# Performance work log

Measured on AMD Instinct MI355X. Metric: run time of the kernel, lower is better.

## Reference

```python
import jax, jax.numpy as jnp
import numpy as np

K = 1024
T = 16384
P = 2          # number of lags
N_STAGES = 2   # len(s_list)
EDGE_P = 0.005 # edge density -> avg degree ~5


def setup_inputs() -> dict:
    key = jax.random.key(0)
    kX, kA, ka, kb0, kb1 = jax.random.split(key, 5)
    X = jax.random.normal(kX, (K, T), dtype=jnp.float32)
    # sparse symmetric 0/1 adjacency, zero diagonal
    U = jax.random.uniform(kA, (K, K))
    Ab = (U < EDGE_P)
    Ab = (Ab | Ab.T) & ~jnp.eye(K, dtype=bool)
    A = Ab.astype(jnp.float32)
    alpha = jax.random.normal(ka, (P,), dtype=jnp.float32)
    beta0 = jax.random.normal(kb0, (P,), dtype=jnp.float32)
    beta1 = jax.random.normal(kb1, (P,), dtype=jnp.float32)
    return {"X": X, "A": A, "alpha": alpha, "beta0": beta0, "beta1": beta1}


def _stage_avg_matrices(A):
    """M[r] averages over nodes at shortest-path distance exactly r+1 (rows with
    no stage-r neighbors are all-zero, matching the `if neighbors:` guard)."""
    Ab = A > 0.5
    Af = Ab.astype(jnp.float32)
    reach_prev = jnp.eye(A.shape[0], dtype=bool)  # distance <= 0
    Ms = []
    for _ in range(N_STAGES):
        reach = reach_prev | ((reach_prev.astype(jnp.float32) @ Af) > 0.5)
        exact = reach & ~reach_prev                     # distance == r+1
        exact_f = exact.astype(jnp.float32)
        deg = exact_f.sum(axis=1, keepdims=True)        # (K, 1)
        M = exact_f / jnp.maximum(deg, 1.0)             # zero rows stay zero
        Ms.append(M)
        reach_prev = reach
    return Ms


def reference(X, A, alpha, beta0, beta1):
    K_, T_ = X.shape
    betas = [beta0, beta1]
    Ms = _stage_avg_matrices(A)
    # one dense aggregation per stage over ALL time steps, then slice lags
    MXs = [M @ X for M in Ms]                           # each (K, T)
    Y = jnp.zeros((K_, T_ - P), dtype=X.dtype)
    for lag in range(1, P + 1):
        sl = slice(P - lag, T_ - lag)
        Y = Y + alpha[lag - 1] * X[:, sl]
        for stage in range(N_STAGES):
            Y = Y + betas[stage][lag - 1] * MXs[stage][:, sl]
    return Y
```

## Files before the change

kernel.cpp:

```cpp
#include <hip/hip_runtime.h>

typedef float fx4 __attribute__((ext_vector_type(4)));
typedef short s16x8 __attribute__((ext_vector_type(8)));
typedef __bf16 bfx8 __attribute__((ext_vector_type(8)));

#define KN 1024
#define TT 16384
#define NOUT 16382
#define NKT 32
#define COLP 16640
#define HLDS 49216

#define APK_OFF 34078720u
#define B1_OFF  (APK_OFF + 4194304u)

__device__ __forceinline__ unsigned short f2bf(float f) {
  return __builtin_bit_cast(unsigned short, (__bf16)f);
}

__device__ __forceinline__ void gll16(const void* g, void* l) {
  __builtin_amdgcn_global_load_lds(
      (const __attribute__((address_space(1))) void*)g,
      (__attribute__((address_space(3))) void*)l, 16, 0, 0);
}

__global__ __launch_bounds__(256) void k_masks(const float* __restrict__ A,
                                               unsigned* __restrict__ B1) {
  int k = blockIdx.x;
  int tid = threadIdx.x;
  int wv = tid >> 6, lane = tid & 63;
  for (int i = 0; i < 4; ++i) {
    int n = i * 256 + wv * 64 + lane;
    bool bit = (A[(size_t)k * KN + n] > 0.5f) && (n != k);
    unsigned long long m = __ballot(bit);
    if (lane == 0) {
      B1[k * 32 + i * 8 + wv * 2]     = (unsigned)m;
      B1[k * 32 + i * 8 + wv * 2 + 1] = (unsigned)(m >> 32);
    }
  }
}

__global__ __launch_bounds__(256) void k_wp(const unsigned* __restrict__ B1,
                                            const float* __restrict__ alpha,
                                            const float* __restrict__ beta0,
                                            const float* __restrict__ beta1,
                                            const float* __restrict__ X,
                                            unsigned short* __restrict__ Wc,
                                            unsigned short* __restrict__ Xbf) {
  int tid = threadIdx.x;
  if (blockIdx.x >= 1024) {
    int p = blockIdx.x - 1024;
    int o = p & 127;
    int cb = p >> 7;
    int c = cb * 256 + tid;
    unsigned v[4];
#pragma unroll
    for (int q = 0; q < 4; ++q) {
      float f0 = 0.f, f1 = 0.f;
      if (c < TT) {
        f0 = X[(size_t)(o * 8 + q * 2) * TT + c];
        f1 = X[(size_t)(o * 8 + q * 2 + 1) * TT + c];
      }
      v[q] = (unsigned)f2bf(f0) | ((unsigned)f2bf(f1) << 16);
    }
    uint4 w; w.x = v[0]; w.y = v[1]; w.z = v[2]; w.w = v[3];
    *reinterpret_cast<uint4*>(Xbf + ((size_t)o * COLP + c) * 8) = w;
    return;
  }
  __shared__ unsigned reach[32];
  __shared__ unsigned ex2[32];
  __shared__ unsigned short list[1056];
  __shared__ int nl;
  int k = blockIdx.x;
  if (tid == 0) nl = 0;
  if (tid < 32) {
    unsigned r = B1[k * 32 + tid];
    if (tid == (k >> 5)) r |= 1u << (k & 31);
    reach[tid] = r;
    ex2[tid] = 0;
  }
  __syncthreads();
  for (int m = tid; m < KN; m += 256)
    if ((reach[m >> 5] >> (m & 31)) & 1) {
      int i = atomicAdd(&nl, 1);
      list[i] = (unsigned short)m;
    }
  __syncthreads();
  int n2 = nl;
  for (int i = 0; i < n2; ++i) {
    int m = list[i];
    if (tid < 32) ex2[tid] |= B1[m * 32 + tid];
  }
  __syncthreads();
  if (tid < 32) ex2[tid] &= ~reach[tid];
  __syncthreads();
  int d1 = 0, d2 = 0;
  for (int w = 0; w < 32; ++w) { d1 += __popc(reach[w]); d2 += __popc(ex2[w]); }
  d1 -= 1;
  float rd1 = 1.0f / fmaxf((float)d1, 1.0f);
  float rd2 = 1.0f / fmaxf((float)d2, 1.0f);
  float c00 = beta0[0] * rd1, c01 = beta0[1] * rd1;
  float c10 = beta1[0] * rd2, c11 = beta1[1] * rd2;
  float a0 = alpha[0], a1 = alpha[1];
  int mb = k >> 8, rloc = k & 255;
  for (int q = 0; q < 4; ++q) {
    int n = tid * 4 + q;
    bool in1 = (((reach[n >> 5] >> (n & 31)) & 1) != 0) && (n != k);
    bool in2 = ((ex2[n >> 5] >> (n & 31)) & 1) != 0;
    float v0 = (in1 ? c00 : 0.f) + (in2 ? c10 : 0.f) + (n == k ? a0 : 0.f);
    float v1 = (in1 ? c01 : 0.f) + (in2 ? c11 : 0.f) + (n == k ? a1 : 0.f);
    int t = n >> 5, kb2 = (n >> 3) & 3, ii = n & 7;
    size_t base = (size_t)mb * 524288 + (size_t)t * 16384 +
                  kb2 * 2048 + rloc * 8 + ii;
    Wc[base] = f2bf(v0);
    Wc[base + 8192] = f2bf(v1);
  }
}

__global__ __launch_bounds__(512, 2) void k_gemm(const char* __restrict__ Apk,
                                                 const char* __restrict__ Xbf,
                                                 float* __restrict__ Y) {
  __shared__ __align__(16) char lds[2 * HLDS];
  int bid = blockIdx.x;
  int swz = (bid & 7) * 32 + (bid >> 3);
  int jb = swz >> 2, mb = swz & 3;
  int tid = threadIdx.x;
  int lane = tid & 63, wv = tid >> 6;
  int wm = wv >> 2, wn = wv & 3;
  int fl = (wv >> 2) & 1;
  int kb = lane >> 4, ml = lane & 15;
  const char* Asrc = Apk + (size_t)mb * 1048576;

  fx4 acc[2][4][4];
#pragma unroll
  for (int q = 0; q < 2; ++q)
#pragma unroll
    for (int a = 0; a < 4; ++a)
#pragma unroll
      for (int b = 0; b < 4; ++b) acc[q][a][b] = (fx4){0.f, 0.f, 0.f, 0.f};

  auto stageA = [&](int t) {
    char* dst = lds + (t & 1) * HLDS;
    const char* src = Asrc + (size_t)(t & (NKT - 1)) * 32768;
#pragma unroll
    for (int u = 0; u < 4; ++u)
      gll16(src + tid * 16 + u * 8192, dst + tid * 16 + u * 8192);
  };
  auto stageB = [&](int t) {
    char* dstB = lds + (t & 1) * HLDS + 32768;
    int ts = t & (NKT - 1);
#pragma unroll
    for (int u2 = 0; u2 < 2; ++u2) {
      int u = tid + u2 * 512;
      const char* src = Xbf +
          ((size_t)(ts * 4 + (u >> 8)) * COLP + jb * 256 + (u & 255)) * 16;
      gll16(src, dstB + u * 16);
    }
    if (tid < 4) {
      const char* src = Xbf +
          ((size_t)(ts * 4 + tid) * COLP + jb * 256 + 256) * 16;
      gll16(src, dstB + 16384);
    }
  };

#define READ_A(dst, t, s, qm)                                                       \
  do {                                                                              \
    const char* Ah_ = lds + ((t) & 1) * HLDS + (s) * 16384;                         \
    _Pragma("unroll") for (int mf = 0; mf < 4; ++mf)                                \
      dst[mf] = *(const s16x8*)(Ah_ +                                               \
          (size_t)(kb * 256 + wm * 128 + (qm) * 64 + mf * 16 + ml) * 16);           \
  } while (0)
#define READ_B(dst, t, off)                                                         \
  do {                                                                              \
    const char* Bh_ = lds + ((t) & 1) * HLDS + 32768;                               \
    _Pragma("unroll") for (int nf = 0; nf < 4; ++nf) {                              \
      int c_ = wn * 64 + nf * 16 + ml + (off);                                      \
      const char* a_ = Bh_ + (size_t)(kb * 256 + c_) * 16;                          \
      if ((off) == 1 && nf == 3) {                                                  \
        if (c_ == 256) a_ = Bh_ + 16384 + kb * 16;                                  \
      }                                                                             \
      dst[nf] = *(const s16x8*)a_;                                                  \
    }                                                                               \
  } while (0)
#define MFMA16(acc_, a_, b_)                                                        \
  do {                                                                              \
    __builtin_amdgcn_s_setprio(1);                                                  \
    _Pragma("unroll") for (int mf = 0; mf < 4; ++mf)                                \
      _Pragma("unroll") for (int nf = 0; nf < 4; ++nf)                              \
        acc_[mf][nf] = __builtin_amdgcn_mfma_f32_16x16x32_bf16(                     \
            __builtin_bit_cast(bfx8, a_[mf]), __builtin_bit_cast(bfx8, b_[nf]),     \
            acc_[mf][nf], 0, 0, 0);                                                 \
    __builtin_amdgcn_s_setprio(0);                                                  \
  } while (0)

#define S_PASS(s, DO_STAGE)                                                         \
  do {                                                                              \
    READ_B(bA, kt, 1 - (s));                                                        \
    READ_A(aA, kt, s, 0);                                                           \
    if (DO_STAGE) stageA(kt + 1);                                                   \
    MFMA16(acc[0], aA, bA);                                                         \
    READ_A(aB, kt, s, 1);                                                           \
    if (DO_STAGE) stageB(kt + 1);                                                   \
    MFMA16(acc[1], aB, bA);                                                         \
  } while (0)

  s16x8 aA[4], aB[4], bA[4];

  stageA(0); stageB(0);
  asm volatile("s_waitcnt vmcnt(0)" ::: "memory");
  __builtin_amdgcn_s_barrier();

  for (int kt = 0; kt < NKT; ++kt) {
    if (fl == 0) {
      S_PASS(0, 1);
      S_PASS(1, 0);
    } else {
      S_PASS(1, 1);
      S_PASS(0, 0);
    }
    asm volatile("s_waitcnt vmcnt(0)" ::: "memory");
    __builtin_amdgcn_s_barrier();
  }

  int c0 = jb * 256 + wn * 64;
  int r0 = mb * 256 + wm * 128;
#pragma unroll
  for (int qm = 0; qm < 2; ++qm)
#pragma unroll
    for (int mf = 0; mf < 4; ++mf)
#pragma unroll
      for (int nf = 0; nf < 4; ++nf) {
        int c = c0 + nf * 16 + ml;
        if (c < NOUT) {
          int r = r0 + qm * 64 + mf * 16 + (lane >> 4) * 4;
#pragma unroll
          for (int i = 0; i < 4; ++i)
            Y[(size_t)(r + i) * NOUT + c] = acc[qm][mf][nf][i];
        }
      }
#undef READ_A
#undef READ_B
#undef MFMA16
#undef S_PASS
}

extern "C" void kernel_launch(void* const* d_in, const int* in_sizes, int n_in,
                              void* d_out, int out_size, void* d_ws, size_t ws_size,
                              hipStream_t stream) {
  const float* X     = (const float*)d_in[0];
  const float* A     = (const float*)d_in[1];
  const float* alpha = (const float*)d_in[2];
  const float* beta0 = (const float*)d_in[3];
  const float* beta1 = (const float*)d_in[4];
  float* Y = (float*)d_out;
  char* ws = (char*)d_ws;
  char* Xbf = ws;
  char* Apk = ws + APK_OFF;
  unsigned* B1 = (unsigned*)(ws + B1_OFF);

  k_masks<<<dim3(1024), dim3(256), 0, stream>>>(A, B1);
  k_wp<<<dim3(9344), dim3(256), 0, stream>>>(B1, alpha, beta0, beta1, X,
                                             (unsigned short*)Apk,
                                             (unsigned short*)Xbf);
  k_gemm<<<dim3(256), dim3(512), 0, stream>>>(Apk, Xbf, Y);
}
```

Measured before the change: 83.96 us.

## Halve GEMM M-tile to 128 rows with 256-thread blocks and 512 workgroups

Restructures the GEMM tiling: each workgroup now covers 128 output rows instead of 256, using 4 waves instead of 8, and the grid doubles to 512 blocks. Each wave computes a 64x128 tile with 32 accumulators, and the staggered two-pass schedule is replaced by a simple uniform pass order. Shared memory per block shrinks, which allows more resident blocks and better CU fill on a 256-CU device. The cost is that each X tile is loaded by twice as many blocks, and the simpler schedule may overlap LDS reads with MFMA less well.

```diff
diff --git a/kernel.cpp b/kernel.cpp
--- a/kernel.cpp
+++ b/kernel.cpp
@@ -9,7 +9,7 @@
 #define NOUT 16382
 #define NKT 32
 #define COLP 16640
-#define HLDS 49216
+#define HLDS 32832
 
 #define APK_OFF 34078720u
 #define B1_OFF  (APK_OFF + 4194304u)
@@ -117,41 +117,44 @@
   }
 }
 
-__global__ __launch_bounds__(512, 2) void k_gemm(const char* __restrict__ Apk,
+__global__ __launch_bounds__(256, 2) void k_gemm(const char* __restrict__ Apk,
                                                  const char* __restrict__ Xbf,
                                                  float* __restrict__ Y) {
   __shared__ __align__(16) char lds[2 * HLDS];
   int bid = blockIdx.x;
-  int swz = (bid & 7) * 32 + (bid >> 3);
-  int jb = swz >> 2, mb = swz & 3;
+  int swz = (bid & 7) * 64 + (bid >> 3);
+  int jb = swz >> 3, mb = swz & 7;
+  int mb4 = mb >> 1, half = mb & 1;
   int tid = threadIdx.x;
   int lane = tid & 63, wv = tid >> 6;
-  int wm = wv >> 2, wn = wv & 3;
-  int fl = (wv >> 2) & 1;
+  int wm = wv >> 1, wn = wv & 1;
   int kb = lane >> 4, ml = lane & 15;
-  const char* Asrc = Apk + (size_t)mb * 1048576;
-
-  fx4 acc[2][4][4];
-#pragma unroll
-  for (int q = 0; q < 2; ++q)
-#pragma unroll
-    for (int a = 0; a < 4; ++a)
-#pragma unroll
-      for (int b = 0; b < 4; ++b) acc[q][a][b] = (fx4){0.f, 0.f, 0.f, 0.f};
+  const char* Asrc = Apk + (size_t)mb4 * 524288 * 2;
+
+  fx4 acc[4][8];
+#pragma unroll
+  for (int a = 0; a < 4; ++a)
+#pragma unroll
+    for (int b = 0; b < 8; ++b) acc[a][b] = (fx4){0.f, 0.f, 0.f, 0.f};
 
   auto stageA = [&](int t) {
     char* dst = lds + (t & 1) * HLDS;
-    const char* src = Asrc + (size_t)(t & (NKT - 1)) * 32768;
-#pragma unroll
-    for (int u = 0; u < 4; ++u)
-      gll16(src + tid * 16 + u * 8192, dst + tid * 16 + u * 8192);
+    int ts = t & (NKT - 1);
+#pragma unroll
+    for (int q = 0; q < 4; ++q) {
+      int u = tid + q * 256;
+      int s_ = u >> 9, kb_ = (u >> 7) & 3, r_ = u & 127;
+      const char* src = Asrc + (size_t)ts * 32768 + s_ * 16384 + kb_ * 4096 +
+                        (half * 128 + r_) * 16;
+      gll16(src, dst + u * 16);
+    }
   };
   auto stageB = [&](int t) {
-    char* dstB = lds + (t & 1) * HLDS + 32768;
+    char* dstB = lds + (t & 1) * HLDS + 16384;
     int ts = t & (NKT - 1);
 #pragma unroll
-    for (int u2 = 0; u2 < 2; ++u2) {
-      int u = tid + u2 * 512;
+    for (int u2 = 0; u2 < 4; ++u2) {
+      int u = tid + u2 * 256;
       const char* src = Xbf +
           ((size_t)(ts * 4 + (u >> 8)) * COLP + jb * 256 + (u & 255)) * 16;
       gll16(src, dstB + u * 16);
@@ -163,85 +166,72 @@
     }
   };
 
-#define READ_A(dst, t, s, qm)                                                       \
+#define READ_A(dst, t, s)                                                           \
   do {                                                                              \
-    const char* Ah_ = lds + ((t) & 1) * HLDS + (s) * 16384;                         \
+    const char* Ah_ = lds + ((t) & 1) * HLDS + (s) * 8192;                          \
     _Pragma("unroll") for (int mf = 0; mf < 4; ++mf)                                \
       dst[mf] = *(const s16x8*)(Ah_ +                                               \
-          (size_t)(kb * 256 + wm * 128 + (qm) * 64 + mf * 16 + ml) * 16);           \
+          (size_t)(kb * 128 + wm * 64 + mf * 16 + ml) * 16);                        \
   } while (0)
 #define READ_B(dst, t, off)                                                         \
   do {                                                                              \
-    const char* Bh_ = lds + ((t) & 1) * HLDS + 32768;                               \
-    _Pragma("unroll") for (int nf = 0; nf < 4; ++nf) {                              \
-      int c_ = wn * 64 + nf * 16 + ml + (off);                                      \
+    const char* Bh_ = lds + ((t) & 1) * HLDS + 16384;                               \
+    _Pragma("unroll") for (int nf = 0; nf < 8; ++nf) {                              \
+      int c_ = wn * 128 + nf * 16 + ml + (off);                                     \
       const char* a_ = Bh_ + (size_t)(kb * 256 + c_) * 16;                          \
-      if ((off) == 1 && nf == 3) {                                                  \
+      if ((off) == 1 && nf == 7) {                                                  \
         if (c_ == 256) a_ = Bh_ + 16384 + kb * 16;                                  \
       }                                                                             \
       dst[nf] = *(const s16x8*)a_;                                                  \
     }                                                                               \
   } while (0)
-#define MFMA16(acc_, a_, b_)                                                        \
+#define MFMA32(a_, b_)                                                              \
   do {                                                                              \
     __builtin_amdgcn_s_setprio(1);                                                  \
     _Pragma("unroll") for (int mf = 0; mf < 4; ++mf)                                \
-      _Pragma("unroll") for (int nf = 0; nf < 4; ++nf)                              \
-        acc_[mf][nf] = __builtin_amdgcn_mfma_f32_16x16x32_bf16(                     \
+      _Pragma("unroll") for (int nf = 0; nf < 8; ++nf)                              \
+        acc[mf][nf] = __builtin_amdgcn_mfma_f32_16x16x32_bf16(                      \
             __builtin_bit_cast(bfx8, a_[mf]), __builtin_bit_cast(bfx8, b_[nf]),     \
-            acc_[mf][nf], 0, 0, 0);                                                 \
+            acc[mf][nf], 0, 0, 0);                                                  \
     __builtin_amdgcn_s_setprio(0);                                                  \
   } while (0)
 
-#define S_PASS(s, DO_STAGE)                                                         \
-  do {                                                                              \
-    READ_B(bA, kt, 1 - (s));                                                        \
-    READ_A(aA, kt, s, 0);                                                           \
-    if (DO_STAGE) stageA(kt + 1);                                                   \
-    MFMA16(acc[0], aA, bA);                                                         \
-    READ_A(aB, kt, s, 1);                                                           \
-    if (DO_STAGE) stageB(kt + 1);                                                   \
-    MFMA16(acc[1], aB, bA);                                                         \
-  } while (0)
-
-  s16x8 aA[4], aB[4], bA[4];
+  s16x8 aA[4], bA[8];
 
   stageA(0); stageB(0);
   asm volatile("s_waitcnt vmcnt(0)" ::: "memory");
   __builtin_amdgcn_s_barrier();
 
   for (int kt = 0; kt < NKT; ++kt) {
-    if (fl == 0) {
-      S_PASS(0, 1);
-      S_PASS(1, 0);
-    } else {
-      S_PASS(1, 1);
-      S_PASS(0, 0);
-    }
+    READ_B(bA, kt, 1);
+    READ_A(aA, kt, 0);
+    stageA(kt + 1);
+    MFMA32(aA, bA);
+    READ_B(bA, kt, 0);
+    READ_A(aA, kt, 1);
+    stageB(kt + 1);
+    MFMA32(aA, bA);
     asm volatile("s_waitcnt vmcnt(0)" ::: "memory");
     __builtin_amdgcn_s_barrier();
   }
 
-  int c0 = jb * 256 + wn * 64;
-  int r0 = mb * 256 + wm * 128;
-#pragma unroll
-  for (int qm = 0; qm < 2; ++qm)
-#pragma unroll
-    for (int mf = 0; mf < 4; ++mf)
-#pragma unroll
-      for (int nf = 0; nf < 4; ++nf) {
-        int c = c0 + nf * 16 + ml;
-        if (c < NOUT) {
-          int r = r0 + qm * 64 + mf * 16 + (lane >> 4) * 4;
-#pragma unroll
-          for (int i = 0; i < 4; ++i)
-            Y[(size_t)(r + i) * NOUT + c] = acc[qm][mf][nf][i];
-        }
+  int c0 = jb * 256 + wn * 128;
+  int r0 = mb * 128 + wm * 64;
+#pragma unroll
+  for (int mf = 0; mf < 4; ++mf)
+#pragma unroll
+    for (int nf = 0; nf < 8; ++nf) {
+      int c = c0 + nf * 16 + ml;
+      if (c < NOUT) {
+        int r = r0 + mf * 16 + (lane >> 4) * 4;
+#pragma unroll
+        for (int i = 0; i < 4; ++i)
+          Y[(size_t)(r + i) * NOUT + c] = acc[mf][nf][i];
       }
+    }
 #undef READ_A
 #undef READ_B
-#undef MFMA16
-#undef S_PASS
+#undef MFMA32
 }
 
 extern "C" void kernel_launch(void* const* d_in, const int* in_sizes, int n_in,
@@ -262,5 +252,5 @@
   k_wp<<<dim3(9344), dim3(256), 0, stream>>>(B1, alpha, beta0, beta1, X,
                                              (unsigned short*)Apk,
                                              (unsigned short*)Xbf);
-  k_gemm<<<dim3(256), dim3(512), 0, stream>>>(Apk, Xbf, Y);
-}
+  k_gemm<<<dim3(512), dim3(256), 0, stream>>>(Apk, Xbf, Y);
+}
```

Measured after the change: 81.37 us. -3.1%, faster.
